# Kernel tuning notes

Hardware: AMD Instinct MI355X
Metric: run time of the kernel (lower is better)

The kernel has to match this reference:

```python
import jax, jax.numpy as jnp
import numpy as np
import math

M = 4096   # mem_dim == hidden_size (required: C @ qt)
D = 2048   # input_size


def setup_inputs() -> dict:
    key = jax.random.key(0)
    ks = jax.random.split(key, 16)
    f = lambda k, s: jax.random.normal(k, s, dtype=jnp.float32)
    return {
        "x": f(ks[0], (D, 1)),
        "cp": f(ks[1], (M, M)),
        "n_prev": f(ks[2], (M, 1)),
        "Wq": f(ks[3], (M, D)),
        "bq": f(ks[4], (M, 1)),
        "Wk": f(ks[5], (M, D)),
        "bk": f(ks[6], (M, 1)),
        "Wv": f(ks[7], (M, D)),
        "bV": f(ks[8], (M, 1)),
        "Wi": f(ks[9], (1, D)),
        "bi": f(ks[10], (1,)),
        "Wf": f(ks[11], (1, D)),
        "bf": f(ks[12], (1,)),
        "Wo": f(ks[13], (1, D)),
        "bo": f(ks[14], (1,)),
    }


def reference(x, cp, n_prev, Wq, bq, Wk, bk, Wv, bV, Wi, bi, Wf, bf, Wo, bo):
    inv_sqrt_m = 1.0 / math.sqrt(M)
    qt = Wq @ x + bq                      # (M, 1)
    kt = inv_sqrt_m * (Wk @ x + bk)       # (M, 1)
    vt = Wv @ x + bV                      # (M, 1)
    it = jnp.exp(Wi @ x + bi)             # (1, 1) input gate (exp)
    ft = jnp.exp(Wf @ x + bf)             # (1, 1) forget gate (exp)
    v = vt[:, 0]                          # (M,)
    k = kt[:, 0]                          # (M,)
    # matrix memory update: C = f*C_prev + i * v k^T
    C = ft * cp + it * jnp.outer(v, k)    # (M, M)
    n = ft * n_prev + it * k[:, None]     # (M, 1)
    denom = jnp.maximum(jnp.abs(n.T @ qt), 1.0)   # (1, 1)
    h_tilde = (C @ qt) / denom            # (M, 1)
    ot = jax.nn.sigmoid(Wo @ x + bo)      # (1, 1)
    ht = ot * h_tilde                     # (M, 1)
    return (ht, C, n)
```

## Files before the change

### kernel.cpp

```cpp
#include <hip/hip_runtime.h>
#include <math.h>

#define MM 4096
#define DD 2048


__global__ __launch_bounds__(256) void k1_gemv_gates(
    const float* __restrict__ x,
    const float* __restrict__ Wq, const float* __restrict__ bq,
    const float* __restrict__ Wk, const float* __restrict__ bk,
    const float* __restrict__ Wv, const float* __restrict__ bV,
    const float* __restrict__ Wi, const float* __restrict__ bi,
    const float* __restrict__ Wf, const float* __restrict__ bf,
    const float* __restrict__ Wo, const float* __restrict__ bo,
    float* __restrict__ ws)
{
    const int lane = threadIdx.x & 63;
    const int wid  = threadIdx.x >> 6;

    if (blockIdx.x >= 1024) {
        __shared__ double gred[4];
        const int g = blockIdx.x - 1024;
        const float* G = (g == 0) ? Wi : ((g == 1) ? Wf : Wo);
        const float4* g4 = (const float4*)G;
        const float4* xv = (const float4*)x;
        double acc = 0.0;
        for (int t = threadIdx.x; t < DD / 4; t += 256) {
            float4 gg = g4[t];
            float4 xx = xv[t];
            acc += (double)gg.x * xx.x + (double)gg.y * xx.y
                 + (double)gg.z * xx.z + (double)gg.w * xx.w;
        }
        for (int off = 32; off; off >>= 1) acc += __shfl_down(acc, off, 64);
        if (lane == 0) gred[wid] = acc;
        __syncthreads();
        if (threadIdx.x == 0) {
            double s = gred[0] + gred[1] + gred[2] + gred[3];
            if (g == 0)      ws[3 * MM + 0] = (float)exp(s + (double)bi[0]);
            else if (g == 1) ws[3 * MM + 1] = (float)exp(s + (double)bf[0]);
            else             ws[3 * MM + 2] = (float)(1.0 / (1.0 + exp(-(s + (double)bo[0]))));
        }
        return;
    }

    __shared__ float xs[DD];
    {
        const float4* xv  = (const float4*)x;
        float4*       xsv = (float4*)xs;
        xsv[threadIdx.x]       = xv[threadIdx.x];
        xsv[256 + threadIdx.x] = xv[256 + threadIdx.x];
    }
    __syncthreads();

    const int row = blockIdx.x * 4 + wid;
    const float4* wq = (const float4*)(Wq + (size_t)row * DD);
    const float4* wk = (const float4*)(Wk + (size_t)row * DD);
    const float4* wv = (const float4*)(Wv + (size_t)row * DD);

    float4 rq[8], rk[8], rv[8];
    #pragma unroll
    for (int t = 0; t < 8; ++t) rq[t] = wq[lane + 64 * t];
    #pragma unroll
    for (int t = 0; t < 8; ++t) rk[t] = wk[lane + 64 * t];
    #pragma unroll
    for (int t = 0; t < 8; ++t) rv[t] = wv[lane + 64 * t];

    const float4* xs4 = (const float4*)xs;
    float aq = 0.f, ak = 0.f, av = 0.f;
    #pragma unroll
    for (int t = 0; t < 8; ++t) {
        float4 xx = xs4[lane + 64 * t];
        aq += rq[t].x * xx.x + rq[t].y * xx.y + rq[t].z * xx.z + rq[t].w * xx.w;
        ak += rk[t].x * xx.x + rk[t].y * xx.y + rk[t].z * xx.z + rk[t].w * xx.w;
        av += rv[t].x * xx.x + rv[t].y * xx.y + rv[t].z * xx.z + rv[t].w * xx.w;
    }
    for (int off = 32; off; off >>= 1) {
        aq += __shfl_down(aq, off, 64);
        ak += __shfl_down(ak, off, 64);
        av += __shfl_down(av, off, 64);
    }
    if (lane == 0) {
        ws[row]          = aq + bq[row];
        ws[MM + row]     = (ak + bk[row]) * (1.0f / 64.0f);
        ws[2 * MM + row] = av + bV[row];
    }
}

__global__ __launch_bounds__(256) void k2_rowC(
    const float* __restrict__ cp, const float* __restrict__ n_prev,
    float* __restrict__ ws, float* __restrict__ C_out, float* __restrict__ n_out)
{
    __shared__ float ks[MM];
    __shared__ float qs[MM];
    __shared__ float sred[16];
    const int lane = threadIdx.x & 63;
    const int wid  = threadIdx.x >> 6;

    const float it = ws[3 * MM + 0];
    const float ft = ws[3 * MM + 1];

    if (blockIdx.x == 0) {
        const float4* np4 = (const float4*)n_prev;
        const float4* kv4 = (const float4*)(ws + MM);
        const float4* qv4 = (const float4*)ws;
        float4* n4 = (float4*)n_out;
        float acc = 0.f;
        #pragma unroll
        for (int j = 0; j < MM / 4 / 256; ++j) {
            int t = threadIdx.x + 256 * j;
            float4 np = np4[t], kk = kv4[t], qq = qv4[t];
            float4 nn;
            nn.x = fmaf(ft, np.x, it * kk.x);
            nn.y = fmaf(ft, np.y, it * kk.y);
            nn.z = fmaf(ft, np.z, it * kk.z);
            nn.w = fmaf(ft, np.w, it * kk.w);
            n4[t] = nn;
            acc += nn.x * qq.x + nn.y * qq.y + nn.z * qq.z + nn.w * qq.w;
        }
        for (int off = 32; off; off >>= 1) acc += __shfl_down(acc, off, 64);
        if (lane == 0) sred[wid] = acc;
        __syncthreads();
        if (threadIdx.x == 0) {
            float s = sred[0] + sred[1] + sred[2] + sred[3];
            ws[3 * MM + 3] = fmaxf(fabsf(s), 1.0f);
        }
        __syncthreads();
    }

    {
        const float4* kv4 = (const float4*)(ws + MM);
        const float4* qv4 = (const float4*)ws;
        float4* ks4 = (float4*)ks;
        float4* qs4 = (float4*)qs;
        #pragma unroll
        for (int j = 0; j < MM / 4 / 256; ++j) {
            int t = threadIdx.x + 256 * j;
            ks4[t] = kv4[t];
            qs4[t] = qv4[t];
        }
    }
    __syncthreads();

    const float4* ks4 = (const float4*)ks;
    const float4* qs4 = (const float4*)qs;
    float rowacc[4];
    #pragma unroll
    for (int j = 0; j < 4; ++j) {
        const int row = blockIdx.x * 4 + j;
        const float ivi = it * ws[2 * MM + row];
        const float4* cprow = (const float4*)(cp + (size_t)row * MM);
        float4*       crow  = (float4*)(C_out + (size_t)row * MM);
        float acc = 0.f;
        #pragma unroll
        for (int u = 0; u < MM / 4 / 256; ++u) {
            int t = threadIdx.x + 256 * u;
            float4 c = cprow[t], kk = ks4[t], qq = qs4[t];
            float4 o;
            o.x = fmaf(ivi, kk.x, ft * c.x);
            o.y = fmaf(ivi, kk.y, ft * c.y);
            o.z = fmaf(ivi, kk.z, ft * c.z);
            o.w = fmaf(ivi, kk.w, ft * c.w);
            crow[t] = o;
            acc += o.x * qq.x + o.y * qq.y + o.z * qq.z + o.w * qq.w;
        }
        rowacc[j] = acc;
    }
    __syncthreads();
    #pragma unroll
    for (int j = 0; j < 4; ++j) {
        float acc = rowacc[j];
        for (int off = 32; off; off >>= 1) acc += __shfl_down(acc, off, 64);
        if (lane == 0) sred[j * 4 + wid] = acc;
    }
    __syncthreads();
    if (threadIdx.x < 4) {
        int j = threadIdx.x;
        float s = sred[j * 4 + 0] + sred[j * 4 + 1] + sred[j * 4 + 2] + sred[j * 4 + 3];
        ws[4 * MM + blockIdx.x * 4 + j] = s;
    }
}

__global__ __launch_bounds__(256) void k3_finalize(
    const float* __restrict__ ws, float* __restrict__ ht_out)
{
    const float ot    = ws[3 * MM + 2];
    const float denom = ws[3 * MM + 3];
    const int i = blockIdx.x * 256 + threadIdx.x;
    ht_out[i] = ot * (ws[4 * MM + i] / denom);
}

extern "C" void kernel_launch(void* const* d_in, const int* in_sizes, int n_in,
                              void* d_out, int out_size, void* d_ws, size_t ws_size,
                              hipStream_t stream)
{
    const float* x      = (const float*)d_in[0];
    const float* cp     = (const float*)d_in[1];
    const float* n_prev = (const float*)d_in[2];
    const float* Wq = (const float*)d_in[3];
    const float* bq = (const float*)d_in[4];
    const float* Wk = (const float*)d_in[5];
    const float* bk = (const float*)d_in[6];
    const float* Wv = (const float*)d_in[7];
    const float* bV = (const float*)d_in[8];
    const float* Wi = (const float*)d_in[9];
    const float* bi = (const float*)d_in[10];
    const float* Wf = (const float*)d_in[11];
    const float* bf = (const float*)d_in[12];
    const float* Wo = (const float*)d_in[13];
    const float* bo = (const float*)d_in[14];

    float* out = (float*)d_out;
    float* ht  = out;
    float* C   = out + MM;
    float* n   = out + MM + (size_t)MM * MM;
    float* ws  = (float*)d_ws;

    k1_gemv_gates<<<1027, 256, 0, stream>>>(x, Wq, bq, Wk, bk, Wv, bV,
                                            Wi, bi, Wf, bf, Wo, bo, ws);
    k2_rowC      <<<1024, 256, 0, stream>>>(cp, n_prev, ws, C, n);
    k3_finalize  <<<MM / 256, 256, 0, stream>>>(ws, ht);
}
```

Measured before the change: 232.0 us.

## Use one block per C row, drop LDS staging, add nontemporal C stores

Rewrites the C-update kernel to use one block per row (4097 blocks) instead of four rows per block. The k and q vectors are now read straight from global memory/L2 into registers instead of being staged into 32 KB of shared memory. The n update and denominator move to an extra block that no longer stalls block 0. C is written with nontemporal stores to reduce cache pollution. Meant to raise occupancy and memory-level parallelism on the bandwidth-bound 64 MB read plus 64 MB write, at the cost of redundant k and q reads per block.

Result: no change. 229.6 us (-1.0%).

```diff
diff --git a/kernel.cpp b/kernel.cpp
--- a/kernel.cpp
+++ b/kernel.cpp
@@ -3,6 +3,8 @@
 
 #define MM 4096
 #define DD 2048
+
+typedef float floatx4 __attribute__((ext_vector_type(4)));
 
 
 __global__ __launch_bounds__(256) void k1_gemv_gates(
@@ -90,24 +92,21 @@
     const float* __restrict__ cp, const float* __restrict__ n_prev,
     float* __restrict__ ws, float* __restrict__ C_out, float* __restrict__ n_out)
 {
-    __shared__ float ks[MM];
-    __shared__ float qs[MM];
-    __shared__ float sred[16];
     const int lane = threadIdx.x & 63;
     const int wid  = threadIdx.x >> 6;
 
-    const float it = ws[3 * MM + 0];
-    const float ft = ws[3 * MM + 1];
-
-    if (blockIdx.x == 0) {
+    if (blockIdx.x == MM) {
+        __shared__ float pred[4];
+        const float it = ws[3 * MM + 0];
+        const float ft = ws[3 * MM + 1];
         const float4* np4 = (const float4*)n_prev;
         const float4* kv4 = (const float4*)(ws + MM);
         const float4* qv4 = (const float4*)ws;
         float4* n4 = (float4*)n_out;
         float acc = 0.f;
         #pragma unroll
-        for (int j = 0; j < MM / 4 / 256; ++j) {
-            int t = threadIdx.x + 256 * j;
+        for (int u = 0; u < 4; ++u) {
+            int t = threadIdx.x + 256 * u;
             float4 np = np4[t], kk = kv4[t], qq = qv4[t];
             float4 nn;
             nn.x = fmaf(ft, np.x, it * kk.x);
@@ -118,66 +117,51 @@
             acc += nn.x * qq.x + nn.y * qq.y + nn.z * qq.z + nn.w * qq.w;
         }
         for (int off = 32; off; off >>= 1) acc += __shfl_down(acc, off, 64);
-        if (lane == 0) sred[wid] = acc;
+        if (lane == 0) pred[wid] = acc;
         __syncthreads();
         if (threadIdx.x == 0) {
-            float s = sred[0] + sred[1] + sred[2] + sred[3];
+            float s = pred[0] + pred[1] + pred[2] + pred[3];
             ws[3 * MM + 3] = fmaxf(fabsf(s), 1.0f);
         }
-        __syncthreads();
-    }
-
-    {
-        const float4* kv4 = (const float4*)(ws + MM);
-        const float4* qv4 = (const float4*)ws;
-        float4* ks4 = (float4*)ks;
-        float4* qs4 = (float4*)qs;
-        #pragma unroll
-        for (int j = 0; j < MM / 4 / 256; ++j) {
-            int t = threadIdx.x + 256 * j;
-            ks4[t] = kv4[t];
-            qs4[t] = qv4[t];
-        }
-    }
+        return;
+    }
+
+    __shared__ float sred[4];
+    const int row = blockIdx.x;
+    const float it  = ws[3 * MM + 0];
+    const float ft  = ws[3 * MM + 1];
+    const float ivi = it * ws[2 * MM + row];
+
+    const float4* cprow = (const float4*)(cp + (size_t)row * MM);
+    const float4* kv4   = (const float4*)(ws + MM);
+    const float4* qv4   = (const float4*)ws;
+    float4*       crow  = (float4*)(C_out + (size_t)row * MM);
+
+    float4 c[4], kk[4], qq[4];
+    #pragma unroll
+    for (int u = 0; u < 4; ++u) c[u]  = cprow[threadIdx.x + 256 * u];
+    #pragma unroll
+    for (int u = 0; u < 4; ++u) kk[u] = kv4[threadIdx.x + 256 * u];
+    #pragma unroll
+    for (int u = 0; u < 4; ++u) qq[u] = qv4[threadIdx.x + 256 * u];
+
+    float acc = 0.f;
+    #pragma unroll
+    for (int u = 0; u < 4; ++u) {
+        float4 o;
+        o.x = fmaf(ivi, kk[u].x, ft * c[u].x);
+        o.y = fmaf(ivi, kk[u].y, ft * c[u].y);
+        o.z = fmaf(ivi, kk[u].z, ft * c[u].z);
+        o.w = fmaf(ivi, kk[u].w, ft * c[u].w);
+        floatx4 ov = { o.x, o.y, o.z, o.w };
+        __builtin_nontemporal_store(ov, (floatx4*)(crow + threadIdx.x + 256 * u));
+        acc += o.x * qq[u].x + o.y * qq[u].y + o.z * qq[u].z + o.w * qq[u].w;
+    }
+    for (int off = 32; off; off >>= 1) acc += __shfl_down(acc, off, 64);
+    if (lane == 0) sred[wid] = acc;
     __syncthreads();
-
-    const float4* ks4 = (const float4*)ks;
-    const float4* qs4 = (const float4*)qs;
-    float rowacc[4];
-    #pragma unroll
-    for (int j = 0; j < 4; ++j) {
-        const int row = blockIdx.x * 4 + j;
-        const float ivi = it * ws[2 * MM + row];
-        const float4* cprow = (const float4*)(cp + (size_t)row * MM);
-        float4*       crow  = (float4*)(C_out + (size_t)row * MM);
-        float acc = 0.f;
-        #pragma unroll
-        for (int u = 0; u < MM / 4 / 256; ++u) {
-            int t = threadIdx.x + 256 * u;
-            float4 c = cprow[t], kk = ks4[t], qq = qs4[t];
-            float4 o;
-            o.x = fmaf(ivi, kk.x, ft * c.x);
-            o.y = fmaf(ivi, kk.y, ft * c.y);
-            o.z = fmaf(ivi, kk.z, ft * c.z);
-            o.w = fmaf(ivi, kk.w, ft * c.w);
-            crow[t] = o;
-            acc += o.x * qq.x + o.y * qq.y + o.z * qq.z + o.w * qq.w;
-        }
-        rowacc[j] = acc;
-    }
-    __syncthreads();
-    #pragma unroll
-    for (int j = 0; j < 4; ++j) {
-        float acc = rowacc[j];
-        for (int off = 32; off; off >>= 1) acc += __shfl_down(acc, off, 64);
-        if (lane == 0) sred[j * 4 + wid] = acc;
-    }
-    __syncthreads();
-    if (threadIdx.x < 4) {
-        int j = threadIdx.x;
-        float s = sred[j * 4 + 0] + sred[j * 4 + 1] + sred[j * 4 + 2] + sred[j * 4 + 3];
-        ws[4 * MM + blockIdx.x * 4 + j] = s;
-    }
+    if (threadIdx.x == 0)
+        ws[4 * MM + row] = sred[0] + sred[1] + sred[2] + sred[3];
 }
 
 __global__ __launch_bounds__(256) void k3_finalize(
@@ -217,6 +201,6 @@
 
     k1_gemv_gates<<<1027, 256, 0, stream>>>(x, Wq, bq, Wk, bk, Wv, bV,
                                             Wi, bi, Wf, bf, Wo, bo, ws);
-    k2_rowC      <<<1024, 256, 0, stream>>>(cp, n_prev, ws, C, n);
+    k2_rowC      <<<MM + 1, 256, 0, stream>>>(cp, n_prev, ws, C, n);
     k3_finalize  <<<MM / 256, 256, 0, stream>>>(ws, ht);
 }
```
